# Optimization experiments

Measured on AMD Instinct MI355X. Metric: run time of the kernel, lower is better.

## Reference

```python
import jax, jax.numpy as jnp
import numpy as np

B, SEQ, DIM = 2, 2048, 1024
HEADS, DIM_HEAD = 16, 64
INNER = HEADS * DIM_HEAD
SCALE = DIM_HEAD ** -0.5


def rotate_half(x):
    # pair consecutive dims (d r) with r=2: (x1, x2) -> (-x2, x1)
    xp = x.reshape(*x.shape[:-1], -1, 2)
    x1, x2 = xp[..., 0], xp[..., 1]
    return jnp.stack((-x2, x1), axis=-1).reshape(x.shape)


def apply_rotary_emb(freqs, t):
    # freqs: [n, rot_dim] angles; t: [b, h, n, d]
    rot_dim = freqs.shape[-1]
    t_rot, t_pass = t[..., :rot_dim], t[..., rot_dim:]
    t_rot = t_rot * jnp.cos(freqs) + rotate_half(t_rot) * jnp.sin(freqs)
    return jnp.concatenate([t_rot, t_pass], axis=-1)


def setup_inputs() -> dict:
    key = jax.random.key(0)
    ks = jax.random.split(key, 4)
    x = jax.random.normal(ks[0], (B, SEQ, DIM), dtype=jnp.float32)
    mask = jnp.ones((B, SEQ), dtype=bool)
    rotary_pos_emb = jax.random.uniform(ks[1], (SEQ, DIM_HEAD), dtype=jnp.float32)
    Wqkv = jax.random.normal(ks[2], (DIM, 3 * INNER), dtype=jnp.float32) * 0.02
    Wout = jax.random.normal(ks[3], (INNER, DIM), dtype=jnp.float32) * 0.02
    bout = jnp.zeros((DIM,), dtype=jnp.float32)
    return {"x": x, "mask": mask, "rotary_pos_emb": rotary_pos_emb,
            "Wqkv": Wqkv, "Wout": Wout, "bout": bout}


def reference(x, mask, rotary_pos_emb, Wqkv, Wout, bout):
    b, n, _ = x.shape
    qkv = x @ Wqkv                                   # [b, n, 3*inner]
    q, k, v = jnp.split(qkv, 3, axis=-1)

    def to_heads(t):
        return t.reshape(b, n, HEADS, DIM_HEAD).transpose(0, 2, 1, 3)  # [b,h,n,d]

    q, k, v = to_heads(q), to_heads(k), to_heads(v)
    freqs = rotary_pos_emb[:n, :]
    # NB: original applies rotary to q, k AND v
    q = apply_rotary_emb(freqs, q)
    k = apply_rotary_emb(freqs, k)
    v = apply_rotary_emb(freqs, v)
    q = q * SCALE

    dots = jnp.einsum('bhid,bhjd->bhij', q, k)       # [b,h,n,n]
    mask_value = -jnp.finfo(dots.dtype).max
    pad = mask[:, None, None, :]                     # [b,1,1,n] keep where True
    dots = jnp.where(pad, dots, mask_value)
    idx = jnp.arange(n)
    causal = idx[None, :] > idx[:, None]             # j >= i + (j-i+1) with i==j==n
    dots = jnp.where(causal[None, None], mask_value, dots)

    attn = jax.nn.softmax(dots, axis=-1)
    out = jnp.einsum('bhij,bhjd->bhid', attn, v)     # [b,h,n,d]
    out = out.transpose(0, 2, 1, 3).reshape(b, n, INNER)
    return out @ Wout + bout
```

## Files before the change

### kernel.cpp

```cpp
#include <hip/hip_runtime.h>
#include <hip/hip_bf16.h>
#include <stdint.h>

#define DEVI __device__ __forceinline__

typedef __bf16 bf16x8 __attribute__((ext_vector_type(8)));
typedef float f32x4 __attribute__((ext_vector_type(4)));
typedef float f32x16 __attribute__((ext_vector_type(16)));

static constexpr int SEQ = 2048;
static constexpr int DIM = 1024;
static constexpr int HEADS = 16;
static constexpr int NQKV = 3072;
static constexpr int MROWS = 4096;
static constexpr float QSCALE = 0.125f;
static constexpr float LOG2E = 1.4426950408889634f;

DEVI unsigned short f2bf(float f) {
  unsigned int u = __builtin_bit_cast(unsigned int, f);
  u += 0x7FFFu + ((u >> 16) & 1u);
  return (unsigned short)(u >> 16);
}

DEVI bf16x8 ld8(const unsigned short* p) {
  return __builtin_bit_cast(bf16x8, *(const uint4*)p);
}

DEVI f32x4 mfma16(bf16x8 a, bf16x8 b, f32x4 c) {
  return __builtin_amdgcn_mfma_f32_16x16x32_bf16(a, b, c, 0, 0, 0);
}

DEVI f32x16 mfma32(bf16x8 a, bf16x8 b, f32x16 c) {
  return __builtin_amdgcn_mfma_f32_32x32x16_bf16(a, b, c, 0, 0, 0);
}

DEVI void load_lds16(const void* g, void* l) {
  __builtin_amdgcn_global_load_lds((const __attribute__((address_space(1))) void*)g,
                                   (__attribute__((address_space(3))) void*)l,
                                   16, 0, 0);
}

DEVI int swz(int row, int kelem) {
  return row * 64 + (kelem ^ ((row & 7) << 3));
}

DEVI unsigned cvtpk(float lo, float hi) {
  unsigned r;
  asm("v_cvt_pk_bf16_f32 %0, %1, %2" : "=v"(r) : "v"(lo), "v"(hi));
  return r;
}

DEVI void pl32swap(unsigned& a, unsigned& b) {
  asm volatile("v_permlane32_swap_b32 %0, %1" : "+v"(a), "+v"(b));
}
DEVI float xhalf_max(float v) { return fmaxf(v, __shfl_xor(v, 32)); }
DEVI float xhalf_sum(float v) { return v + __shfl_xor(v, 32); }

__global__ __launch_bounds__(256) void k_rope_tables(const float* __restrict__ rope,
                                                     float* __restrict__ cosb,
                                                     float* __restrict__ sinb) {
  int i = blockIdx.x * 256 + threadIdx.x;
  float f = rope[i];
  cosb[i] = cosf(f);
  sinb[i] = sinf(f);
}

__global__ __launch_bounds__(256) void k_cast_bf16(const float* __restrict__ in,
                                                   unsigned short* __restrict__ out) {
  int i = blockIdx.x * 256 + threadIdx.x;
  float4 f = *(const float4*)(in + (size_t)i * 4);
  ushort4 v;
  v.x = f2bf(f.x); v.y = f2bf(f.y); v.z = f2bf(f.z); v.w = f2bf(f.w);
  *(ushort4*)(out + (size_t)i * 4) = v;
}

__global__ __launch_bounds__(256) void k_transpose_bf16(const float* __restrict__ in,
                                                        unsigned short* __restrict__ out,
                                                        int Kd, int Nd) {
  __shared__ unsigned short T[64][68];
  const int n0 = blockIdx.x * 64, k0 = blockIdx.y * 64;
  const int rr = threadIdx.x >> 4, cc = (threadIdx.x & 15) * 4;
#pragma unroll
  for (int p = 0; p < 4; ++p) {
    const int r = p * 16 + rr;
    float4 f = *(const float4*)(in + (size_t)(k0 + r) * Nd + n0 + cc);
    T[r][cc + 0] = f2bf(f.x);
    T[r][cc + 1] = f2bf(f.y);
    T[r][cc + 2] = f2bf(f.z);
    T[r][cc + 3] = f2bf(f.w);
  }
  __syncthreads();
#pragma unroll
  for (int p = 0; p < 4; ++p) {
    const int rn = p * 16 + rr;
    ushort4 v;
    v.x = T[cc + 0][rn];
    v.y = T[cc + 1][rn];
    v.z = T[cc + 2][rn];
    v.w = T[cc + 3][rn];
    *(ushort4*)(out + (size_t)(n0 + rn) * Kd + k0 + cc) = v;
  }
}

DEVI void gemm_mainloop(const unsigned short* __restrict__ A,
                        const unsigned short* __restrict__ B, int K,
                        int m0, int n0,
                        unsigned short* As, unsigned short* Bs,
                        f32x4 (&acc)[4][4]) {
  const int lane = threadIdx.x & 63;
  const int wid = threadIdx.x >> 6;
  const int wm = wid >> 1, wn = wid & 1;
  for (int kt = 0; kt < K; kt += 32) {
    __syncthreads();
#pragma unroll
    for (int i = 0; i < 2; ++i) {
      const int chunk = wid * 2 + i;
      const int row = chunk * 16 + (lane >> 2);
      const int kc = kt + (lane & 3) * 8;
      load_lds16(A + (size_t)(m0 + row) * K + kc, As + chunk * 512);
      load_lds16(B + (size_t)(n0 + row) * K + kc, Bs + chunk * 512);
    }
    __syncthreads();
    bf16x8 af[4], bfv[4];
#pragma unroll
    for (int mi = 0; mi < 4; ++mi)
      af[mi] = ld8(&As[(wm * 64 + mi * 16 + (lane & 15)) * 32 + 8 * (lane >> 4)]);
#pragma unroll
    for (int ni = 0; ni < 4; ++ni)
      bfv[ni] = ld8(&Bs[(wn * 64 + ni * 16 + (lane & 15)) * 32 + 8 * (lane >> 4)]);
#pragma unroll
    for (int mi = 0; mi < 4; ++mi)
#pragma unroll
      for (int ni = 0; ni < 4; ++ni)
        acc[mi][ni] = mfma16(af[mi], bfv[ni], acc[mi][ni]);
  }
}

__global__ __launch_bounds__(256) void k_gemm_qkv(
    const unsigned short* __restrict__ xb, const unsigned short* __restrict__ wt,
    const float* __restrict__ cosb, const float* __restrict__ sinb,
    unsigned short* __restrict__ qb, unsigned short* __restrict__ kb,
    unsigned short* __restrict__ vb) {
  __shared__ unsigned short As[128 * 32];
  __shared__ unsigned short Bs[128 * 32];
  const int m0 = blockIdx.x * 128, n0 = blockIdx.y * 128;
  f32x4 acc[4][4] = {};
  gemm_mainloop(xb, wt, DIM, m0, n0, As, Bs, acc);
  const int lane = threadIdx.x & 63, wid = threadIdx.x >> 6;
  const int wm = wid >> 1, wn = wid & 1;
#pragma unroll
  for (int mi = 0; mi < 4; ++mi) {
#pragma unroll
    for (int ni = 0; ni < 4; ++ni) {
      const int ng = n0 + wn * 64 + ni * 16 + (lane & 15);
      const int d = ng & 63;
      const int part = ng >> 10;
      const int h = (ng & 1023) >> 6;
#pragma unroll
      for (int r = 0; r < 4; ++r) {
        const int mg = m0 + wm * 64 + mi * 16 + 4 * (lane >> 4) + r;
        const int s = mg & (SEQ - 1), b = mg >> 11;
        float v = acc[mi][ni][r];
        float p = __shfl_xor(v, 1);
        float cv = cosb[(s << 6) + d], sv = sinb[(s << 6) + d];
        float rot = v * cv + ((d & 1) ? p : -p) * sv;
        const size_t bh = (size_t)(b * HEADS + h);
        if (part == 0) {
          qb[(bh * SEQ + s) * 64 + d] = f2bf(rot * (QSCALE * LOG2E));
        } else if (part == 1) {
          kb[(bh * SEQ + s) * 64 + d] = f2bf(rot);
        } else {
          vb[(bh * 64 + d) * SEQ + s] = f2bf(rot);
        }
      }
    }
  }
}

__global__ __launch_bounds__(256) void k_flash(
    const unsigned short* __restrict__ qb, const unsigned short* __restrict__ kb,
    const unsigned short* __restrict__ vtb, unsigned short* __restrict__ ao) {
  __shared__ __align__(16) unsigned short Ks[2][2][64 * 64];
  __shared__ __align__(16) unsigned short Vt[2][2][64 * 64];
  const int bh = blockIdx.x;
  const int j = blockIdx.y;
  const int tid = threadIdx.x, lane = tid & 63, wid = tid >> 6;
  const int wq = wid >> 1, wk = wid & 1;
  const int la31 = lane & 31, h = lane >> 5;
  const unsigned short* kbh = kb + (size_t)bh * SEQ * 64;
  const unsigned short* vbh = vtb + (size_t)bh * 64 * SEQ;
  const int b = bh >> 4, hh = bh & 15;
  const int sslot = ((lane & 7) ^ (lane >> 3)) * 8;
  float* mrg = (float*)&Ks[0][0][0];
  const int mbase = wq * 2176;

  auto stage = [&](int buf, int t) {
    const int kv0 = t * 64;
#pragma unroll
    for (int i = 0; i < 4; ++i) {
      const int chunk = wq * 4 + i;
      const int row = chunk * 8 + (lane >> 3);
      load_lds16(kbh + ((size_t)(kv0 + row) << 6) + sslot, &Ks[buf][wk][chunk * 512]);
      load_lds16(vbh + (size_t)row * SEQ + kv0 + sslot, &Vt[buf][wk][chunk * 512]);
    }
  };

#pragma unroll 1
  for (int hf = 0; hf < 2; ++hf) {
    const int qt = hf == 0 ? (31 - j) : j;
    const int q0 = qt * 64 + wq * 32;
    const int qr = q0 + la31;
    const unsigned short* qp = qb + ((size_t)bh * SEQ + qr) * 64;
    bf16x8 qf0 = ld8(qp + 0 + 8 * h);
    bf16x8 qf1 = ld8(qp + 16 + 8 * h);
    bf16x8 qf2 = ld8(qp + 32 + 8 * h);
    bf16x8 qf3 = ld8(qp + 48 + 8 * h);

    f32x16 o0 = {}, o1 = {};
    float m = -1e30f, l = 0.f;
    const int nkv = qt + 1;
    const int nst = (nkv + 1) >> 1;

    if (wk < nkv) stage(0, wk);
#pragma unroll 1
    for (int st = 0; st < nst; ++st) {
      const int cur = st & 1;
      const int t = 2 * st + wk;
      __syncthreads();
      { const int tn = 2 * (st + 1) + wk; if (tn < nkv) stage(cur ^ 1, tn); }

      if (t < nkv) {
        const int kv0 = t * 64;
        const unsigned short* Kc = &Ks[cur][wk][0];
        const unsigned short* Vc = &Vt[cur][wk][0];
        f32x16 st0 = {}, st1 = {};
        __builtin_amdgcn_s_setprio(1);
#pragma unroll
        for (int ks = 0; ks < 4; ++ks) {
          bf16x8 qk = (ks == 0) ? qf0 : (ks == 1) ? qf1 : (ks == 2) ? qf2 : qf3;
          st0 = mfma32(ld8(&Kc[swz(la31, 16 * ks + 8 * h)]), qk, st0);
          st1 = mfma32(ld8(&Kc[swz(32 + la31, 16 * ks + 8 * h)]), qk, st1);
        }
        __builtin_amdgcn_s_setprio(0);
        if (kv0 + 63 > q0) {
#pragma unroll
          for (int r = 0; r < 16; ++r) {
            const int kvo = (r & 3) + 8 * (r >> 2) + 4 * h;
            st0[r] = (kv0 + kvo > qr) ? -1e30f : st0[r];
            st1[r] = (kv0 + 32 + kvo > qr) ? -1e30f : st1[r];
          }
        }
        float a8[8];
#pragma unroll
        for (int i = 0; i < 8; ++i)
          a8[i] = fmaxf(fmaxf(st0[i], st0[i + 8]), fmaxf(st1[i], st1[i + 8]));
        float a4_0 = fmaxf(a8[0], a8[4]), a4_1 = fmaxf(a8[1], a8[5]);
        float a4_2 = fmaxf(a8[2], a8[6]), a4_3 = fmaxf(a8[3], a8[7]);
        float pmax = fmaxf(fmaxf(a4_0, a4_1), fmaxf(a4_2, a4_3));
        const bool nor = __all(pmax <= m + 8.f);
        float scl = 1.f;
        if (!nor) {
          const float rowmax = xhalf_max(pmax);
          const float mnew = fmaxf(m, rowmax);
          scl = exp2f(m - mnew);
          m = mnew;
        }
#pragma unroll
        for (int r = 0; r < 16; ++r) {
          st0[r] = exp2f(st0[r] - m);
          st1[r] = exp2f(st1[r] - m);
        }
        float s8[8];
#pragma unroll
        for (int i = 0; i < 8; ++i)
          s8[i] = (st0[i] + st0[i + 8]) + (st1[i] + st1[i + 8]);
        float s4_0 = s8[0] + s8[4], s4_1 = s8[1] + s8[5];
        float s4_2 = s8[2] + s8[6], s4_3 = s8[3] + s8[7];
        float psum = (s4_0 + s4_1) + (s4_2 + s4_3);
        const float rowsum = xhalf_sum(psum);
        if (nor) {
          l += rowsum;
        } else {
          l = l * scl + rowsum;
#pragma unroll
          for (int r = 0; r < 16; ++r) { o0[r] *= scl; o1[r] *= scl; }
        }

        unsigned w0 = cvtpk(st0[0], st0[1]),   w1 = cvtpk(st0[2], st0[3]);
        unsigned w2 = cvtpk(st0[4], st0[5]),   w3 = cvtpk(st0[6], st0[7]);
        unsigned w4 = cvtpk(st0[8], st0[9]),   w5 = cvtpk(st0[10], st0[11]);
        unsigned w6 = cvtpk(st0[12], st0[13]), w7 = cvtpk(st0[14], st0[15]);
        pl32swap(w0, w2); pl32swap(w1, w3); pl32swap(w4, w6); pl32swap(w5, w7);
        const bf16x8 pa0 = __builtin_bit_cast(bf16x8, (uint4){w0, w1, w2, w3});
        const bf16x8 pa1 = __builtin_bit_cast(bf16x8, (uint4){w4, w5, w6, w7});
        unsigned x0 = cvtpk(st1[0], st1[1]),   x1 = cvtpk(st1[2], st1[3]);
        unsigned x2 = cvtpk(st1[4], st1[5]),   x3 = cvtpk(st1[6], st1[7]);
        unsigned x4 = cvtpk(st1[8], st1[9]),   x5 = cvtpk(st1[10], st1[11]);
        unsigned x6 = cvtpk(st1[12], st1[13]), x7 = cvtpk(st1[14], st1[15]);
        pl32swap(x0, x2); pl32swap(x1, x3); pl32swap(x4, x6); pl32swap(x5, x7);
        const bf16x8 pa2 = __builtin_bit_cast(bf16x8, (uint4){x0, x1, x2, x3});
        const bf16x8 pa3 = __builtin_bit_cast(bf16x8, (uint4){x4, x5, x6, x7});

        __builtin_amdgcn_s_setprio(1);
        o0 = mfma32(ld8(&Vc[swz(la31, 0 + 8 * h)]), pa0, o0);
        o0 = mfma32(ld8(&Vc[swz(la31, 16 + 8 * h)]), pa1, o0);
        o0 = mfma32(ld8(&Vc[swz(la31, 32 + 8 * h)]), pa2, o0);
        o0 = mfma32(ld8(&Vc[swz(la31, 48 + 8 * h)]), pa3, o0);
        o1 = mfma32(ld8(&Vc[swz(32 + la31, 0 + 8 * h)]), pa0, o1);
        o1 = mfma32(ld8(&Vc[swz(32 + la31, 16 + 8 * h)]), pa1, o1);
        o1 = mfma32(ld8(&Vc[swz(32 + la31, 32 + 8 * h)]), pa2, o1);
        o1 = mfma32(ld8(&Vc[swz(32 + la31, 48 + 8 * h)]), pa3, o1);
        __builtin_amdgcn_s_setprio(0);
      }
    }

    __syncthreads();
    if (wk == 1) {
#pragma unroll
      for (int s = 0; s < 8; ++s) {
        f32x4 c;
        if (s < 4) { c[0]=o0[4*s]; c[1]=o0[4*s+1]; c[2]=o0[4*s+2]; c[3]=o0[4*s+3]; }
        else       { c[0]=o1[4*(s-4)]; c[1]=o1[4*(s-4)+1]; c[2]=o1[4*(s-4)+2]; c[3]=o1[4*(s-4)+3]; }
        *(f32x4*)&mrg[mbase + lane * 32 + 4 * (s ^ (lane & 7))] = c;
      }
      mrg[mbase + 2048 + lane] = m;
      mrg[mbase + 2112 + lane] = l;
    }
    __syncthreads();
    if (wk == 0) {
      const float m1 = mrg[mbase + 2048 + lane];
      const float l1 = mrg[mbase + 2112 + lane];
      const float mM = fmaxf(m, m1);
      const float sc0 = exp2f(m - mM), sc1 = exp2f(m1 - mM);
      const float lt = l * sc0 + l1 * sc1;
      const float rl = __builtin_amdgcn_rcpf(lt);
      unsigned short* aor = ao + ((size_t)(b * SEQ + qr)) * 1024 + hh * 64;
#pragma unroll
      for (int s = 0; s < 8; ++s) {
        f32x4 c = *(const f32x4*)&mrg[mbase + lane * 32 + 4 * (s ^ (lane & 7))];
        float v0, v1, v2, v3;
        if (s < 4) {
          v0 = (o0[4*s]   * sc0 + c[0] * sc1) * rl;
          v1 = (o0[4*s+1] * sc0 + c[1] * sc1) * rl;
          v2 = (o0[4*s+2] * sc0 + c[2] * sc1) * rl;
          v3 = (o0[4*s+3] * sc0 + c[3] * sc1) * rl;
        } else {
          v0 = (o1[4*(s-4)]   * sc0 + c[0] * sc1) * rl;
          v1 = (o1[4*(s-4)+1] * sc0 + c[1] * sc1) * rl;
          v2 = (o1[4*(s-4)+2] * sc0 + c[2] * sc1) * rl;
          v3 = (o1[4*(s-4)+3] * sc0 + c[3] * sc1) * rl;
        }
        uint2 uv;
        uv.x = cvtpk(v0, v1);
        uv.y = cvtpk(v2, v3);
        *(uint2*)(aor + (s < 4 ? 8 * s : 32 + 8 * (s - 4)) + 4 * h) = uv;
      }
    }
    __syncthreads();
  }
}

__global__ __launch_bounds__(256) void k_gemm_out(
    const unsigned short* __restrict__ ao, const unsigned short* __restrict__ wt,
    const float* __restrict__ bout, float* __restrict__ out) {
  __shared__ unsigned short As[128 * 32];
  __shared__ unsigned short Bs[128 * 32];
  const int m0 = blockIdx.x * 128, n0 = blockIdx.y * 128;
  f32x4 acc[4][4] = {};
  gemm_mainloop(ao, wt, DIM, m0, n0, As, Bs, acc);
  const int lane = threadIdx.x & 63, wid = threadIdx.x >> 6;
  const int wm = wid >> 1, wn = wid & 1;
#pragma unroll
  for (int mi = 0; mi < 4; ++mi) {
#pragma unroll
    for (int ni = 0; ni < 4; ++ni) {
      const int ng = n0 + wn * 64 + ni * 16 + (lane & 15);
      const float bn = bout[ng];
#pragma unroll
      for (int r = 0; r < 4; ++r) {
        const int mg = m0 + wm * 64 + mi * 16 + 4 * (lane >> 4) + r;
        out[(size_t)mg * DIM + ng] = acc[mi][ni][r] + bn;
      }
    }
  }
}

extern "C" void kernel_launch(void* const* d_in, const int* in_sizes, int n_in,
                              void* d_out, int out_size, void* d_ws, size_t ws_size,
                              hipStream_t stream) {
  const float* x    = (const float*)d_in[0];
  const float* rope = (const float*)d_in[2];
  const float* Wqkv = (const float*)d_in[3];
  const float* Wout = (const float*)d_in[4];
  const float* bout = (const float*)d_in[5];
  float* out = (float*)d_out;

  char* ws = (char*)d_ws;
  unsigned short* xb    = (unsigned short*)(ws + 0);
  unsigned short* wqkvt = (unsigned short*)(ws + 8388608);
  unsigned short* woutt = (unsigned short*)(ws + 14680064);
  float*          cosb  = (float*)(ws + 16777216);
  float*          sinb  = (float*)(ws + 17301504);
  unsigned short* qbuf  = (unsigned short*)(ws + 17825792);
  unsigned short* kbuf  = (unsigned short*)(ws + 26214400);
  unsigned short* vbuf  = (unsigned short*)(ws + 34603008);
  unsigned short* aob   = (unsigned short*)(ws + 42991616);

  k_rope_tables<<<512, 256, 0, stream>>>(rope, cosb, sinb);
  k_cast_bf16<<<4096, 256, 0, stream>>>(x, xb);
  k_transpose_bf16<<<dim3(48, 16), 256, 0, stream>>>(Wqkv, wqkvt, DIM, NQKV);
  k_transpose_bf16<<<dim3(16, 16), 256, 0, stream>>>(Wout, woutt, DIM, DIM);
  k_gemm_qkv<<<dim3(MROWS / 128, NQKV / 128), 256, 0, stream>>>(xb, wqkvt, cosb, sinb,
                                                                qbuf, kbuf, vbuf);
  k_flash<<<dim3(32, 16), 256, 0, stream>>>(qbuf, kbuf, vbuf, aob);
  k_gemm_out<<<dim3(MROWS / 128, DIM / 128), 256, 0, stream>>>(aob, woutt, bout, out);
}
```

Baseline: 139.9 us.

## Restructure flash attention to 32-row query tiles with 4-way KV split per block

```diff
diff --git a/kernel.cpp b/kernel.cpp
--- a/kernel.cpp
+++ b/kernel.cpp
@@ -177,38 +177,36 @@
   }
 }
 
-__global__ __launch_bounds__(256) void k_flash(
+__global__ __launch_bounds__(256, 4) void k_flash(
     const unsigned short* __restrict__ qb, const unsigned short* __restrict__ kb,
     const unsigned short* __restrict__ vtb, unsigned short* __restrict__ ao) {
-  __shared__ __align__(16) unsigned short Ks[2][2][64 * 64];
-  __shared__ __align__(16) unsigned short Vt[2][2][64 * 64];
+  __shared__ __align__(16) unsigned short LDS[4][4096];
   const int bh = blockIdx.x;
   const int j = blockIdx.y;
-  const int tid = threadIdx.x, lane = tid & 63, wid = tid >> 6;
-  const int wq = wid >> 1, wk = wid & 1;
+  const int tid = threadIdx.x, lane = tid & 63, wk = tid >> 6;
   const int la31 = lane & 31, h = lane >> 5;
   const unsigned short* kbh = kb + (size_t)bh * SEQ * 64;
   const unsigned short* vbh = vtb + (size_t)bh * 64 * SEQ;
   const int b = bh >> 4, hh = bh & 15;
-  const int sslot = ((lane & 7) ^ (lane >> 3)) * 8;
-  float* mrg = (float*)&Ks[0][0][0];
-  const int mbase = wq * 2176;
-
-  auto stage = [&](int buf, int t) {
-    const int kv0 = t * 64;
-#pragma unroll
-    for (int i = 0; i < 4; ++i) {
-      const int chunk = wq * 4 + i;
-      const int row = chunk * 8 + (lane >> 3);
-      load_lds16(kbh + ((size_t)(kv0 + row) << 6) + sslot, &Ks[buf][wk][chunk * 512]);
-      load_lds16(vbh + (size_t)row * SEQ + kv0 + sslot, &Vt[buf][wk][chunk * 512]);
-    }
-  };
+  unsigned short* Kc = &LDS[wk][0];
+  unsigned short* Vc = &LDS[wk][2048];
+  float* scr = (float*)&LDS[0][0];
+
+  int kcon[4], vcon[4];
+#pragma unroll
+  for (int i = 0; i < 4; ++i) {
+    const int p = i * 64 + lane;
+    const int row = p >> 3;
+    const int c8 = (p & 7) ^ (row & 7);
+    kcon[i] = row * 64 + c8 * 8;
+    const int d = 2 * row + (c8 >> 2);
+    vcon[i] = d * SEQ + (c8 & 3) * 8;
+  }
 
 #pragma unroll 1
   for (int hf = 0; hf < 2; ++hf) {
-    const int qt = hf == 0 ? (31 - j) : j;
-    const int q0 = qt * 64 + wq * 32;
+    const int qtp = hf == 0 ? (63 - j) : j;
+    const int q0 = qtp * 32;
     const int qr = q0 + la31;
     const unsigned short* qp = qb + ((size_t)bh * SEQ + qr) * 64;
     bf16x8 qf0 = ld8(qp + 0 + 8 * h);
@@ -218,118 +216,136 @@
 
     f32x16 o0 = {}, o1 = {};
     float m = -1e30f, l = 0.f;
-    const int nkv = qt + 1;
-    const int nst = (nkv + 1) >> 1;
-
-    if (wk < nkv) stage(0, wk);
+    const int nkv = qtp + 1;
+
+    auto stage = [&](int t) {
+      const int kv0 = t * 32;
+#pragma unroll
+      for (int i = 0; i < 4; ++i) {
+        load_lds16(kbh + (size_t)(kv0 * 64 + kcon[i]), Kc + i * 512);
+        load_lds16(vbh + (size_t)(kv0 + vcon[i]), Vc + i * 512);
+      }
+    };
+
+    if (wk < nkv) stage(wk);
 #pragma unroll 1
-    for (int st = 0; st < nst; ++st) {
-      const int cur = st & 1;
-      const int t = 2 * st + wk;
-      __syncthreads();
-      { const int tn = 2 * (st + 1) + wk; if (tn < nkv) stage(cur ^ 1, tn); }
-
-      if (t < nkv) {
-        const int kv0 = t * 64;
-        const unsigned short* Kc = &Ks[cur][wk][0];
-        const unsigned short* Vc = &Vt[cur][wk][0];
-        f32x16 st0 = {}, st1 = {};
-        __builtin_amdgcn_s_setprio(1);
-#pragma unroll
-        for (int ks = 0; ks < 4; ++ks) {
-          bf16x8 qk = (ks == 0) ? qf0 : (ks == 1) ? qf1 : (ks == 2) ? qf2 : qf3;
-          st0 = mfma32(ld8(&Kc[swz(la31, 16 * ks + 8 * h)]), qk, st0);
-          st1 = mfma32(ld8(&Kc[swz(32 + la31, 16 * ks + 8 * h)]), qk, st1);
+    for (int t = wk; t < nkv; t += 4) {
+      asm volatile("s_waitcnt vmcnt(0)" ::: "memory");
+      const int kv0 = t * 32;
+      f32x16 st = {};
+      __builtin_amdgcn_s_setprio(1);
+      st = mfma32(ld8(&Kc[swz(la31, 0 + 8 * h)]), qf0, st);
+      st = mfma32(ld8(&Kc[swz(la31, 16 + 8 * h)]), qf1, st);
+      st = mfma32(ld8(&Kc[swz(la31, 32 + 8 * h)]), qf2, st);
+      st = mfma32(ld8(&Kc[swz(la31, 48 + 8 * h)]), qf3, st);
+      __builtin_amdgcn_s_setprio(0);
+      if (t == qtp) {
+#pragma unroll
+        for (int r = 0; r < 16; ++r) {
+          const int kvo = (r & 3) + 8 * (r >> 2) + 4 * h;
+          st[r] = (kv0 + kvo > qr) ? -1e30f : st[r];
         }
-        __builtin_amdgcn_s_setprio(0);
-        if (kv0 + 63 > q0) {
-#pragma unroll
-          for (int r = 0; r < 16; ++r) {
-            const int kvo = (r & 3) + 8 * (r >> 2) + 4 * h;
-            st0[r] = (kv0 + kvo > qr) ? -1e30f : st0[r];
-            st1[r] = (kv0 + 32 + kvo > qr) ? -1e30f : st1[r];
-          }
-        }
-        float a8[8];
-#pragma unroll
-        for (int i = 0; i < 8; ++i)
-          a8[i] = fmaxf(fmaxf(st0[i], st0[i + 8]), fmaxf(st1[i], st1[i + 8]));
-        float a4_0 = fmaxf(a8[0], a8[4]), a4_1 = fmaxf(a8[1], a8[5]);
-        float a4_2 = fmaxf(a8[2], a8[6]), a4_3 = fmaxf(a8[3], a8[7]);
-        float pmax = fmaxf(fmaxf(a4_0, a4_1), fmaxf(a4_2, a4_3));
-        const bool nor = __all(pmax <= m + 8.f);
-        float scl = 1.f;
-        if (!nor) {
-          const float rowmax = xhalf_max(pmax);
-          const float mnew = fmaxf(m, rowmax);
-          scl = exp2f(m - mnew);
-          m = mnew;
-        }
-#pragma unroll
-        for (int r = 0; r < 16; ++r) {
-          st0[r] = exp2f(st0[r] - m);
-          st1[r] = exp2f(st1[r] - m);
-        }
-        float s8[8];
-#pragma unroll
-        for (int i = 0; i < 8; ++i)
-          s8[i] = (st0[i] + st0[i + 8]) + (st1[i] + st1[i + 8]);
-        float s4_0 = s8[0] + s8[4], s4_1 = s8[1] + s8[5];
-        float s4_2 = s8[2] + s8[6], s4_3 = s8[3] + s8[7];
-        float psum = (s4_0 + s4_1) + (s4_2 + s4_3);
-        const float rowsum = xhalf_sum(psum);
-        if (nor) {
-          l += rowsum;
-        } else {
-          l = l * scl + rowsum;
-#pragma unroll
-          for (int r = 0; r < 16; ++r) { o0[r] *= scl; o1[r] *= scl; }
-        }
-
-        unsigned w0 = cvtpk(st0[0], st0[1]),   w1 = cvtpk(st0[2], st0[3]);
-        unsigned w2 = cvtpk(st0[4], st0[5]),   w3 = cvtpk(st0[6], st0[7]);
-        unsigned w4 = cvtpk(st0[8], st0[9]),   w5 = cvtpk(st0[10], st0[11]);
-        unsigned w6 = cvtpk(st0[12], st0[13]), w7 = cvtpk(st0[14], st0[15]);
-        pl32swap(w0, w2); pl32swap(w1, w3); pl32swap(w4, w6); pl32swap(w5, w7);
-        const bf16x8 pa0 = __builtin_bit_cast(bf16x8, (uint4){w0, w1, w2, w3});
-        const bf16x8 pa1 = __builtin_bit_cast(bf16x8, (uint4){w4, w5, w6, w7});
-        unsigned x0 = cvtpk(st1[0], st1[1]),   x1 = cvtpk(st1[2], st1[3]);
-        unsigned x2 = cvtpk(st1[4], st1[5]),   x3 = cvtpk(st1[6], st1[7]);
-        unsigned x4 = cvtpk(st1[8], st1[9]),   x5 = cvtpk(st1[10], st1[11]);
-        unsigned x6 = cvtpk(st1[12], st1[13]), x7 = cvtpk(st1[14], st1[15]);
-        pl32swap(x0, x2); pl32swap(x1, x3); pl32swap(x4, x6); pl32swap(x5, x7);
-        const bf16x8 pa2 = __builtin_bit_cast(bf16x8, (uint4){x0, x1, x2, x3});
-        const bf16x8 pa3 = __builtin_bit_cast(bf16x8, (uint4){x4, x5, x6, x7});
-
-        __builtin_amdgcn_s_setprio(1);
-        o0 = mfma32(ld8(&Vc[swz(la31, 0 + 8 * h)]), pa0, o0);
-        o0 = mfma32(ld8(&Vc[swz(la31, 16 + 8 * h)]), pa1, o0);
-        o0 = mfma32(ld8(&Vc[swz(la31, 32 + 8 * h)]), pa2, o0);
-        o0 = mfma32(ld8(&Vc[swz(la31, 48 + 8 * h)]), pa3, o0);
-        o1 = mfma32(ld8(&Vc[swz(32 + la31, 0 + 8 * h)]), pa0, o1);
-        o1 = mfma32(ld8(&Vc[swz(32 + la31, 16 + 8 * h)]), pa1, o1);
-        o1 = mfma32(ld8(&Vc[swz(32 + la31, 32 + 8 * h)]), pa2, o1);
-        o1 = mfma32(ld8(&Vc[swz(32 + la31, 48 + 8 * h)]), pa3, o1);
-        __builtin_amdgcn_s_setprio(0);
-      }
-    }
-
-    __syncthreads();
-    if (wk == 1) {
+      }
+      float a8[8];
+#pragma unroll
+      for (int i = 0; i < 8; ++i) a8[i] = fmaxf(st[i], st[i + 8]);
+      float a4_0 = fmaxf(a8[0], a8[4]), a4_1 = fmaxf(a8[1], a8[5]);
+      float a4_2 = fmaxf(a8[2], a8[6]), a4_3 = fmaxf(a8[3], a8[7]);
+      float pmax = fmaxf(fmaxf(a4_0, a4_1), fmaxf(a4_2, a4_3));
+      const bool nor = __all(pmax <= m + 8.f);
+      float scl = 1.f;
+      if (!nor) {
+        const float rowmax = xhalf_max(pmax);
+        const float mnew = fmaxf(m, rowmax);
+        scl = exp2f(m - mnew);
+        m = mnew;
+      }
+#pragma unroll
+      for (int r = 0; r < 16; ++r) st[r] = exp2f(st[r] - m);
+      float s8[8];
+#pragma unroll
+      for (int i = 0; i < 8; ++i) s8[i] = st[i] + st[i + 8];
+      float s4_0 = s8[0] + s8[4], s4_1 = s8[1] + s8[5];
+      float s4_2 = s8[2] + s8[6], s4_3 = s8[3] + s8[7];
+      float psum = (s4_0 + s4_1) + (s4_2 + s4_3);
+      const float rowsum = xhalf_sum(psum);
+      if (nor) {
+        l += rowsum;
+      } else {
+        l = l * scl + rowsum;
+#pragma unroll
+        for (int r = 0; r < 16; ++r) { o0[r] *= scl; o1[r] *= scl; }
+      }
+      unsigned w0 = cvtpk(st[0], st[1]),   w1 = cvtpk(st[2], st[3]);
+      unsigned w2 = cvtpk(st[4], st[5]),   w3 = cvtpk(st[6], st[7]);
+      unsigned w4 = cvtpk(st[8], st[9]),   w5 = cvtpk(st[10], st[11]);
+      unsigned w6 = cvtpk(st[12], st[13]), w7 = cvtpk(st[14], st[15]);
+      pl32swap(w0, w2); pl32swap(w1, w3); pl32swap(w4, w6); pl32swap(w5, w7);
+      const bf16x8 pa0 = __builtin_bit_cast(bf16x8, (uint4){w0, w1, w2, w3});
+      const bf16x8 pa1 = __builtin_bit_cast(bf16x8, (uint4){w4, w5, w6, w7});
+      const int rv = la31 >> 1;
+      const int cb = 32 * (la31 & 1) + 8 * h;
+      __builtin_amdgcn_s_setprio(1);
+      o0 = mfma32(ld8(&Vc[swz(rv, cb)]), pa0, o0);
+      o0 = mfma32(ld8(&Vc[swz(rv, cb + 16)]), pa1, o0);
+      o1 = mfma32(ld8(&Vc[swz(16 + rv, cb)]), pa0, o1);
+      o1 = mfma32(ld8(&Vc[swz(16 + rv, cb + 16)]), pa1, o1);
+      __builtin_amdgcn_s_setprio(0);
+      asm volatile("s_waitcnt lgkmcnt(0)" ::: "memory");
+      __builtin_amdgcn_sched_barrier(0);
+      if (t + 4 < nkv) stage(t + 4);
+    }
+
+    __syncthreads();
+    if (wk >= 2) {
+      float* rg = scr + (wk - 2) * 2176;
 #pragma unroll
       for (int s = 0; s < 8; ++s) {
         f32x4 c;
         if (s < 4) { c[0]=o0[4*s]; c[1]=o0[4*s+1]; c[2]=o0[4*s+2]; c[3]=o0[4*s+3]; }
-        else       { c[0]=o1[4*(s-4)]; c[1]=o1[4*(s-4)+1]; c[2]=o1[4*(s-4)+2]; c[3]=o1[4*(s-4)+3]; }
-        *(f32x4*)&mrg[mbase + lane * 32 + 4 * (s ^ (lane & 7))] = c;
-      }
-      mrg[mbase + 2048 + lane] = m;
-      mrg[mbase + 2112 + lane] = l;
+        else { c[0]=o1[4*(s-4)]; c[1]=o1[4*(s-4)+1]; c[2]=o1[4*(s-4)+2]; c[3]=o1[4*(s-4)+3]; }
+        *(f32x4*)&rg[lane * 32 + 4 * (s ^ (lane & 7))] = c;
+      }
+      rg[2048 + lane] = m;
+      rg[2112 + lane] = l;
+    }
+    __syncthreads();
+    if (wk < 2) {
+      float* rg = scr + wk * 2176;
+      const float m1 = rg[2048 + lane], l1 = rg[2112 + lane];
+      const float mM = fmaxf(m, m1);
+      const float sc0 = exp2f(m - mM), sc1 = exp2f(m1 - mM);
+      m = mM;
+      l = l * sc0 + l1 * sc1;
+#pragma unroll
+      for (int s = 0; s < 8; ++s) {
+        f32x4 c = *(const f32x4*)&rg[lane * 32 + 4 * (s ^ (lane & 7))];
+        if (s < 4) {
+#pragma unroll
+          for (int q = 0; q < 4; ++q) o0[4*s+q] = o0[4*s+q] * sc0 + c[q] * sc1;
+        } else {
+#pragma unroll
+          for (int q = 0; q < 4; ++q) o1[4*(s-4)+q] = o1[4*(s-4)+q] * sc0 + c[q] * sc1;
+        }
+      }
+    }
+    __syncthreads();
+    if (wk == 1) {
+      float* rg = scr;
+#pragma unroll
+      for (int s = 0; s < 8; ++s) {
+        f32x4 c;
+        if (s < 4) { c[0]=o0[4*s]; c[1]=o0[4*s+1]; c[2]=o0[4*s+2]; c[3]=o0[4*s+3]; }
+        else { c[0]=o1[4*(s-4)]; c[1]=o1[4*(s-4)+1]; c[2]=o1[4*(s-4)+2]; c[3]=o1[4*(s-4)+3]; }
+        *(f32x4*)&rg[lane * 32 + 4 * (s ^ (lane & 7))] = c;
+      }
+      rg[2048 + lane] = m;
+      rg[2112 + lane] = l;
     }
     __syncthreads();
     if (wk == 0) {
-      const float m1 = mrg[mbase + 2048 + lane];
-      const float l1 = mrg[mbase + 2112 + lane];
+      float* rg = scr;
+      const float m1 = rg[2048 + lane], l1 = rg[2112 + lane];
       const float mM = fmaxf(m, m1);
       const float sc0 = exp2f(m - mM), sc1 = exp2f(m1 - mM);
       const float lt = l * sc0 + l1 * sc1;
@@ -337,7 +353,7 @@
       unsigned short* aor = ao + ((size_t)(b * SEQ + qr)) * 1024 + hh * 64;
 #pragma unroll
       for (int s = 0; s < 8; ++s) {
-        f32x4 c = *(const f32x4*)&mrg[mbase + lane * 32 + 4 * (s ^ (lane & 7))];
+        f32x4 c = *(const f32x4*)&rg[lane * 32 + 4 * (s ^ (lane & 7))];
         float v0, v1, v2, v3;
         if (s < 4) {
           v0 = (o0[4*s]   * sc0 + c[0] * sc1) * rl;
@@ -412,6 +428,6 @@
   k_transpose_bf16<<<dim3(16, 16), 256, 0, stream>>>(Wout, woutt, DIM, DIM);
   k_gemm_qkv<<<dim3(MROWS / 128, NQKV / 128), 256, 0, stream>>>(xb, wqkvt, cosb, sinb,
                                                                 qbuf, kbuf, vbuf);
-  k_flash<<<dim3(32, 16), 256, 0, stream>>>(qbuf, kbuf, vbuf, aob);
+  k_flash<<<dim3(32, 32), 256, 0, stream>>>(qbuf, kbuf, vbuf, aob);
   k_gemm_out<<<dim3(MROWS / 128, DIM / 128), 256, 0, stream>>>(aob, woutt, bout, out);
 }
```

Result: slower. 143.1 us (+2.3%).
